# Kernel optimization log

Hardware: AMD Instinct MI355X
Metric: run time of the kernel (lower is better)

## Reference

```python
import jax, jax.numpy as jnp
import numpy as np

N_HEAD = 8
N_FEAT = 512
EPS = 1e-6


def _forward(query, Wq, bq, Wk, bk, Wv, bv, Wo, bo):
    # query: (bsz, tgt_len, E). key = value = query (self-attention).
    bsz, tgt_len, E = query.shape
    head_dim = E // N_HEAD
    n = bsz * N_HEAD

    # Faithful to torch: .view((L, N, E)) is a RESHAPE, not a transpose.
    x = query.reshape(tgt_len, bsz, E)

    q = x @ Wq.T + bq
    k = x @ Wk.T + bk
    v = x @ Wv.T + bv

    # relu activation on q, k (act_fun='relu')
    q = jax.nn.relu(q).reshape(tgt_len, n, head_dim).swapaxes(0, 1)  # (n, L, d)
    k = jax.nn.relu(k).reshape(tgt_len, n, head_dim).swapaxes(0, 1)  # (n, L, d)
    v = v.reshape(tgt_len, n, head_dim).swapaxes(0, 1)               # (n, L, d)

    # cos reweighting: weight_index = pi/2 * arange(1, m+1) / m
    m = tgt_len
    idx = (np.pi / 2) * jnp.arange(1, m + 1, dtype=query.dtype) / m  # (L,)
    idx = idx[None, :, None]                                         # (1, L, 1)
    q_ = jnp.concatenate([q * jnp.sin(idx), q * jnp.cos(idx)], axis=-1)  # (n, L, 2d)
    k_ = jnp.concatenate([k * jnp.sin(idx), k * jnp.cos(idx)], axis=-1)  # (n, L, 2d)

    # causal linear attention via cumsum recurrence
    kv = jnp.einsum('nld,nlm->nldm', k_, v)          # (n, L, 2d, d)
    kv_cum = jnp.cumsum(kv, axis=1)                  # (n, L, 2d, d)
    qkv = jnp.einsum('nld,nldm->nlm', q_, kv_cum)    # (n, L, d)
    k_cum = jnp.cumsum(k_, axis=1)                   # (n, L, 2d)
    denom = jnp.clip(jnp.einsum('nld,nld->nl', q_, k_cum), EPS, None)
    attn = qkv / denom[..., None]                    # (n, L, d)

    attn = attn.swapaxes(0, 1).reshape(tgt_len, bsz, E)
    out = attn @ Wo.T + bo
    # Faithful to torch: final .view back to (bsz, tgt_len, E) is a reshape.
    return out.reshape(bsz, tgt_len, N_FEAT)


def setup_inputs() -> dict:
    key = jax.random.key(0)
    ks = jax.random.split(key, 9)
    bsz, L, E = 2, 1024, N_FEAT
    scale = 0.02
    return {
        'query': jax.random.normal(ks[0], (bsz, L, E), dtype=jnp.float32),
        'Wq': jax.random.normal(ks[1], (E, E), dtype=jnp.float32) * scale,
        'bq': jnp.zeros((E,), dtype=jnp.float32),
        'Wk': jax.random.normal(ks[2], (E, E), dtype=jnp.float32) * scale,
        'bk': jnp.zeros((E,), dtype=jnp.float32),
        'Wv': jax.random.normal(ks[3], (E, E), dtype=jnp.float32) * scale,
        'bv': jnp.zeros((E,), dtype=jnp.float32),
        'Wo': jax.random.normal(ks[4], (E, E), dtype=jnp.float32) * scale,
        'bo': jnp.zeros((E,), dtype=jnp.float32),
    }


def reference(query, Wq, bq, Wk, bk, Wv, bv, Wo, bo):
    return _forward(query, Wq, bq, Wk, bk, Wv, bv, Wo, bo)
```

## Files before the change

kernel.cpp:

```cpp
#include <hip/hip_runtime.h>
#include <math.h>

#define LSEQ 1024
#define EDIM 512
#define HD 64
#define CCH 64
#define NCH 16
#define DFEAT 128

typedef unsigned short u16;
typedef short bf16x8 __attribute__((ext_vector_type(8)));
typedef float f32x4 __attribute__((ext_vector_type(4)));

__device__ __forceinline__ u16 f2bf(float f) {
    unsigned u = __float_as_uint(f);
    unsigned r = (u + 0x7fffu + ((u >> 16) & 1u)) >> 16;
    return (u16)r;
}
__device__ __forceinline__ float bf2f(u16 x) {
    return __uint_as_float((unsigned)x << 16);
}
__device__ __forceinline__ void async16(void* lds, const void* g) {
    __builtin_amdgcn_global_load_lds(
        (const __attribute__((address_space(1))) unsigned int*)g,
        (__attribute__((address_space(3))) unsigned int*)lds, 16, 0, 0);
}

__global__ __launch_bounds__(256) void cast_kernel(
    const float* __restrict__ X,  const float* __restrict__ Wq,
    const float* __restrict__ Wk, const float* __restrict__ Wv,
    const float* __restrict__ Wo, u16* __restrict__ Xb, u16* __restrict__ Wb)
{
    int i = blockIdx.x * 256 + threadIdx.x;
    const float* src; u16* dst; int off;
    if (i < 262144)      { src = X;  dst = Xb;          off = i; }
    else if (i < 327680) { src = Wq; dst = Wb;          off = i - 262144; }
    else if (i < 393216) { src = Wk; dst = Wb + 262144; off = i - 327680; }
    else if (i < 458752) { src = Wv; dst = Wb + 524288; off = i - 393216; }
    else                 { src = Wo; dst = Wb + 786432; off = i - 458752; }
    float4 v = *(const float4*)&src[(size_t)off * 4];
    ushort4 o; o.x = f2bf(v.x); o.y = f2bf(v.y); o.z = f2bf(v.z); o.w = f2bf(v.w);
    *(ushort4*)&dst[(size_t)off * 4] = o;
}

__global__ __launch_bounds__(256) void qkv_mfma_kernel(
    const u16* __restrict__ Xb, const u16* __restrict__ Wb,
    const float* __restrict__ bq, const float* __restrict__ bk, const float* __restrict__ bv,
    u16* __restrict__ qf, u16* __restrict__ kf, u16* __restrict__ vf)
{
    const int z = blockIdx.z;
    const u16* __restrict__ W = Wb + (size_t)z * 262144;
    const float* __restrict__ bias = (z == 0) ? bq : (z == 1) ? bk : bv;
    const int r0 = blockIdx.x * 128;
    const int j0 = blockIdx.y * 64;
    __shared__ u16 As[128 * 32];
    __shared__ u16 Bs[64 * 32];
    const int t = threadIdx.x;
    const int wave = t >> 6, lane = t & 63;
    const int cl = lane & 15, rg4 = lane >> 4;
    f32x4 acc[2][4];
    #pragma unroll
    for (int ri = 0; ri < 2; ++ri)
        #pragma unroll
        for (int cj = 0; cj < 4; ++cj) acc[ri][cj] = (f32x4){0.f, 0.f, 0.f, 0.f};

    for (int kb = 0; kb < 512; kb += 32) {
        #pragma unroll
        for (int i = 0; i < 2; ++i) {
            int chunk = i * 256 + t;
            int row = chunk >> 2, kg = chunk & 3;
            async16(&As[(i * 256 + wave * 64) * 8], Xb + (size_t)(r0 + row) * 512 + kb + kg * 8);
        }
        {
            int row = t >> 2, kg = t & 3;
            async16(&Bs[(wave * 64) * 8], W + (size_t)(j0 + row) * 512 + kb + kg * 8);
        }
        __syncthreads();
        bf16x8 af[2], bg[4];
        #pragma unroll
        for (int ri = 0; ri < 2; ++ri)
            af[ri] = *(const bf16x8*)&As[(wave * 32 + ri * 16 + cl) * 32 + rg4 * 8];
        #pragma unroll
        for (int cj = 0; cj < 4; ++cj)
            bg[cj] = *(const bf16x8*)&Bs[(cj * 16 + cl) * 32 + rg4 * 8];
        #pragma unroll
        for (int ri = 0; ri < 2; ++ri)
            #pragma unroll
            for (int cj = 0; cj < 4; ++cj)
                acc[ri][cj] = __builtin_amdgcn_mfma_f32_16x16x32_bf16(af[ri], bg[cj], acc[ri][cj], 0, 0, 0);
        __syncthreads();
    }

    float biasv[4];
    #pragma unroll
    for (int cj = 0; cj < 4; ++cj) biasv[cj] = bias[j0 + cj * 16 + cl];
    const int h = j0 >> 6;
    #pragma unroll
    for (int ri = 0; ri < 2; ++ri) {
        #pragma unroll
        for (int rr = 0; rr < 4; ++rr) {
            const int row_g = r0 + wave * 32 + ri * 16 + rg4 * 4 + rr;
            const int l = row_g >> 1, bb = row_g & 1;
            if (z < 2) {
                float ang = 1.5707963267948966f * (float)(l + 1) * (1.0f / 1024.0f);
                float sv, cv;
                sincosf(ang, &sv, &cv);
                u16* __restrict__ dst = (z == 0) ? qf : kf;
                size_t base = (size_t)((bb * 8 + h) * LSEQ + l) * DFEAT;
                #pragma unroll
                for (int cj = 0; cj < 4; ++cj) {
                    const int d = cj * 16 + cl;
                    float y = fmaxf(acc[ri][cj][rr] + biasv[cj], 0.f);
                    dst[base + d]      = f2bf(y * sv);
                    dst[base + d + 64] = f2bf(y * cv);
                }
            } else {
                size_t base = (size_t)((bb * 8 + h) * LSEQ + l) * HD;
                #pragma unroll
                for (int cj = 0; cj < 4; ++cj) {
                    const int d = cj * 16 + cl;
                    vf[base + d] = f2bf(acc[ri][cj][rr] + biasv[cj]);
                }
            }
        }
    }
}

__global__ __launch_bounds__(256) void chunk_sum_kernel(
    const u16* __restrict__ kf, const u16* __restrict__ vf,
    u16* __restrict__ KVc, float* __restrict__ K1c)
{
    const int n = blockIdx.x >> 4;
    const int c = blockIdx.x & 15;
    __shared__ u16 Ks[64 * 128];
    __shared__ u16 KT[128 * 68];
    __shared__ u16 Vs[64 * 64];
    __shared__ u16 VT[64 * 68];
    const int t = threadIdx.x;
    const int wave = t >> 6, lane = t & 63;
    const int cl = lane & 15, rg4 = lane >> 4;
    const u16* kbase = kf + (size_t)(n * LSEQ + c * CCH) * DFEAT;
    const u16* vbase = vf + (size_t)(n * LSEQ + c * CCH) * HD;
    #pragma unroll
    for (int i = 0; i < 4; ++i)
        async16(&Ks[(i * 256 + wave * 64) * 8], kbase + (size_t)(i * 256 + t) * 8);
    #pragma unroll
    for (int i = 0; i < 2; ++i)
        async16(&Vs[(i * 256 + wave * 64) * 8], vbase + (size_t)(i * 256 + t) * 8);
    __syncthreads();
    {
        int m = t & 63, l0 = (t >> 6) * 16;
        #pragma unroll
        for (int half = 0; half < 2; ++half) {
            u16 tmp[8];
            #pragma unroll
            for (int j = 0; j < 8; ++j) tmp[j] = Vs[(l0 + half * 8 + j) * 64 + m];
            *(bf16x8*)&VT[m * 68 + l0 + half * 8] = *(bf16x8*)tmp;
        }
    }
    {
        int d = t & 127, l0 = (t >> 7) * 32;
        #pragma unroll
        for (int q = 0; q < 4; ++q) {
            u16 tmp[8];
            #pragma unroll
            for (int j = 0; j < 8; ++j) tmp[j] = Ks[(l0 + q * 8 + j) * 128 + d];
            *(bf16x8*)&KT[d * 68 + l0 + q * 8] = *(bf16x8*)tmp;
        }
    }
    __syncthreads();
    bf16x8 af[2];
    #pragma unroll
    for (int ks = 0; ks < 2; ++ks)
        af[ks] = *(const bf16x8*)&VT[(wave * 16 + cl) * 68 + ks * 32 + rg4 * 8];
    u16* kvout = KVc + (size_t)(n * NCH + c) * (HD * DFEAT);
    #pragma unroll
    for (int dt = 0; dt < 8; ++dt) {
        f32x4 acc = (f32x4){0.f, 0.f, 0.f, 0.f};
        #pragma unroll
        for (int ks = 0; ks < 2; ++ks) {
            bf16x8 bfr = *(const bf16x8*)&KT[(dt * 16 + cl) * 68 + ks * 32 + rg4 * 8];
            acc = __builtin_amdgcn_mfma_f32_16x16x32_bf16(af[ks], bfr, acc, 0, 0, 0);
        }
        #pragma unroll
        for (int r = 0; r < 4; ++r)
            kvout[(size_t)(wave * 16 + rg4 * 4 + r) * 128 + dt * 16 + cl] = f2bf(acc[r]);
    }
    if (t < 128) {
        float s = 0.f;
        #pragma unroll
        for (int g = 0; g < 8; ++g) {
            bf16x8 kv = *(const bf16x8*)&KT[t * 68 + g * 8];
            #pragma unroll
            for (int j = 0; j < 8; ++j) s += bf2f(((u16*)&kv)[j]);
        }
        K1c[(size_t)(n * NCH + c) * DFEAT + t] = s;
    }
}

__global__ __launch_bounds__(256) void prefix_kernel(
    const u16* __restrict__ KVc, const float* __restrict__ K1c,
    u16* __restrict__ Spt, float* __restrict__ K1p)
{
    const int b = blockIdx.x, t = threadIdx.x;
    const int n = b >> 5;
    const int e = (b & 31) * 256 + t;
    const u16* src = KVc + (size_t)n * NCH * 8192 + e;
    u16* dst = Spt + (size_t)n * NCH * 8192 + e;
    float v[NCH];
    #pragma unroll
    for (int cc = 0; cc < NCH; ++cc) v[cc] = bf2f(src[(size_t)cc * 8192]);
    float run = 0.f;
    #pragma unroll
    for (int cc = 0; cc < NCH; ++cc) { dst[(size_t)cc * 8192] = f2bf(run); run += v[cc]; }
    if (b < 8) {
        const int idx = b * 256 + t;
        const int nn = idx >> 7, d = idx & 127;
        const float* s2 = K1c + (size_t)nn * NCH * DFEAT + d;
        float* d2 = K1p + (size_t)nn * NCH * DFEAT + d;
        float v2[NCH];
        #pragma unroll
        for (int cc = 0; cc < NCH; ++cc) v2[cc] = s2[cc * DFEAT];
        float run2 = 0.f;
        #pragma unroll
        for (int cc = 0; cc < NCH; ++cc) { d2[cc * DFEAT] = run2; run2 += v2[cc]; }
    }
}

__global__ __launch_bounds__(256) void attn_kernel(
    const u16* __restrict__ qf, const u16* __restrict__ kf, const u16* __restrict__ vf,
    const u16* __restrict__ Spt, const float* __restrict__ K1p,
    u16* __restrict__ Amb)
{
    const int n = blockIdx.x >> 4;
    const int c = blockIdx.x & 15;
    __shared__ u16 Qs[64 * 136];
    __shared__ u16 Ks[64 * 136];
    __shared__ u16 VT[64 * 68];
    __shared__ u16 Am[64 * 68];
    __shared__ float K1s[128];
    __shared__ float dsum[64];
    __shared__ float qk1[64];
    const int t = threadIdx.x;
    const int wave = t >> 6, lane = t & 63;
    const int cl = lane & 15, rg4 = lane >> 4;

    const u16* qbase = qf + (size_t)(n * LSEQ + c * CCH) * DFEAT;
    const u16* kbase = kf + (size_t)(n * LSEQ + c * CCH) * DFEAT;
    const u16* vbase = vf + (size_t)(n * LSEQ + c * CCH) * HD;
    const u16* spbase = Spt + (size_t)(n * NCH + c) * 8192;

    bf16x8 spf[4][4];
    #pragma unroll
    for (int nj = 0; nj < 4; ++nj)
        #pragma unroll
        for (int ks = 0; ks < 4; ++ks)
            spf[nj][ks] = *(const bf16x8*)&spbase[(nj * 16 + cl) * 128 + ks * 32 + rg4 * 8];

    #pragma unroll
    for (int i = 0; i < 4; ++i) {
        int chunk = i * 256 + t;
        int row = chunk >> 4, c8 = chunk & 15;
        *(bf16x8*)&Qs[row * 136 + c8 * 8] = *(const bf16x8*)&qbase[row * 128 + c8 * 8];
        *(bf16x8*)&Ks[row * 136 + c8 * 8] = *(const bf16x8*)&kbase[row * 128 + c8 * 8];
    }
    {
        #pragma unroll
        for (int half = 0; half < 2; ++half) {
            u16 tmp[8];
            #pragma unroll
            for (int j = 0; j < 8; ++j) tmp[j] = vbase[(wave * 16 + half * 8 + j) * HD + lane];
            *(bf16x8*)&VT[lane * 68 + wave * 16 + half * 8] = *(bf16x8*)tmp;
        }
    }
    if (t < 128) K1s[t] = K1p[(size_t)(n * NCH + c) * DFEAT + t];
    __syncthreads();

    f32x4 a_acc[4];
    #pragma unroll
    for (int nj = 0; nj < 4; ++nj) a_acc[nj] = (f32x4){0.f, 0.f, 0.f, 0.f};
    #pragma unroll
    for (int ks = 0; ks < 4; ++ks) {
        bf16x8 aq = *(const bf16x8*)&Qs[(wave * 16 + cl) * 136 + ks * 32 + rg4 * 8];
        #pragma unroll
        for (int nj = 0; nj < 4; ++nj) {
            bf16x8 bk = *(const bf16x8*)&Ks[(nj * 16 + cl) * 136 + ks * 32 + rg4 * 8];
            a_acc[nj] = __builtin_amdgcn_mfma_f32_16x16x32_bf16(aq, bk, a_acc[nj], 0, 0, 0);
        }
    }
    #pragma unroll
    for (int r = 0; r < 4; ++r) {
        int l_loc = wave * 16 + rg4 * 4 + r;
        float rs = 0.f;
        #pragma unroll
        for (int nj = 0; nj < 4; ++nj) {
            int lp = nj * 16 + cl;
            float v = (lp <= l_loc) ? a_acc[nj][r] : 0.f;
            Am[l_loc * 68 + lp] = f2bf(v);
            rs += v;
        }
        rs += __shfl_xor(rs, 1); rs += __shfl_xor(rs, 2);
        rs += __shfl_xor(rs, 4); rs += __shfl_xor(rs, 8);
        if (cl == 0) dsum[l_loc] = rs;
    }
    {
        int row = wave * 16 + (lane >> 2), seg = lane & 3;
        float s = 0.f;
        #pragma unroll
        for (int j = 0; j < 32; ++j) {
            int d = seg * 32 + j;
            s += bf2f(Qs[row * 136 + d]) * K1s[d];
        }
        s += __shfl_xor(s, 1); s += __shfl_xor(s, 2);
        if (seg == 0) qk1[row] = s;
    }
    __syncthreads();

    f32x4 oacc[4];
    #pragma unroll
    for (int nj = 0; nj < 4; ++nj) oacc[nj] = (f32x4){0.f, 0.f, 0.f, 0.f};
    #pragma unroll
    for (int ks = 0; ks < 4; ++ks) {
        bf16x8 aq = *(const bf16x8*)&Qs[(wave * 16 + cl) * 136 + ks * 32 + rg4 * 8];
        #pragma unroll
        for (int nj = 0; nj < 4; ++nj)
            oacc[nj] = __builtin_amdgcn_mfma_f32_16x16x32_bf16(aq, spf[nj][ks], oacc[nj], 0, 0, 0);
    }
    #pragma unroll
    for (int ks2 = 0; ks2 < 2; ++ks2) {
        bf16x8 aa = *(const bf16x8*)&Am[(wave * 16 + cl) * 68 + ks2 * 32 + rg4 * 8];
        #pragma unroll
        for (int nj = 0; nj < 4; ++nj) {
            bf16x8 bv = *(const bf16x8*)&VT[(nj * 16 + cl) * 68 + ks2 * 32 + rg4 * 8];
            oacc[nj] = __builtin_amdgcn_mfma_f32_16x16x32_bf16(aa, bv, oacc[nj], 0, 0, 0);
        }
    }
    const int bb = n >> 3, h = n & 7;
    #pragma unroll
    for (int r = 0; r < 4; ++r) {
        int l_loc = wave * 16 + rg4 * 4 + r;
        float den = fmaxf(dsum[l_loc] + qk1[l_loc], 1e-6f);
        float inv = 1.0f / den;
        int rrow = (c * CCH + l_loc) * 2 + bb;
        #pragma unroll
        for (int nj = 0; nj < 4; ++nj) {
            int m = nj * 16 + cl;
            Amb[(size_t)rrow * EDIM + h * 64 + m] = f2bf(oacc[nj][r] * inv);
        }
    }
}

__global__ __launch_bounds__(256) void out_mfma_kernel(
    const u16* __restrict__ Amb, const u16* __restrict__ Wob,
    const float* __restrict__ bo, float* __restrict__ out)
{
    const int r0 = blockIdx.x * 64;
    const int j0 = blockIdx.y * 64;
    __shared__ u16 As[64 * 32];
    __shared__ u16 Bs[64 * 32];
    const int t = threadIdx.x;
    const int wave = t >> 6, lane = t & 63;
    const int cl = lane & 15, rg4 = lane >> 4;
    f32x4 acc[4];
    #pragma unroll
    for (int cj = 0; cj < 4; ++cj) acc[cj] = (f32x4){0.f, 0.f, 0.f, 0.f};

    for (int kb = 0; kb < 512; kb += 32) {
        {
            int row = t >> 2, kg = t & 3;
            async16(&As[(wave * 64) * 8], Amb + (size_t)(r0 + row) * 512 + kb + kg * 8);
            async16(&Bs[(wave * 64) * 8], Wob + (size_t)(j0 + row) * 512 + kb + kg * 8);
        }
        __syncthreads();
        bf16x8 af = *(const bf16x8*)&As[(wave * 16 + cl) * 32 + rg4 * 8];
        bf16x8 bg[4];
        #pragma unroll
        for (int cj = 0; cj < 4; ++cj)
            bg[cj] = *(const bf16x8*)&Bs[(cj * 16 + cl) * 32 + rg4 * 8];
        #pragma unroll
        for (int cj = 0; cj < 4; ++cj)
            acc[cj] = __builtin_amdgcn_mfma_f32_16x16x32_bf16(af, bg[cj], acc[cj], 0, 0, 0);
        __syncthreads();
    }

    float bov[4];
    #pragma unroll
    for (int cj = 0; cj < 4; ++cj) bov[cj] = bo[j0 + cj * 16 + cl];
    #pragma unroll
    for (int rr = 0; rr < 4; ++rr) {
        const int row_g = r0 + wave * 16 + rg4 * 4 + rr;
        #pragma unroll
        for (int cj = 0; cj < 4; ++cj)
            out[(size_t)row_g * EDIM + j0 + cj * 16 + cl] = acc[cj][rr] + bov[cj];
    }
}

extern "C" void kernel_launch(void* const* d_in, const int* in_sizes, int n_in,
                              void* d_out, int out_size, void* d_ws, size_t ws_size,
                              hipStream_t stream) {
    const float* X  = (const float*)d_in[0];
    const float* Wq = (const float*)d_in[1]; const float* bq = (const float*)d_in[2];
    const float* Wk = (const float*)d_in[3]; const float* bk = (const float*)d_in[4];
    const float* Wv = (const float*)d_in[5]; const float* bv = (const float*)d_in[6];
    const float* Wo = (const float*)d_in[7]; const float* bo = (const float*)d_in[8];
    float* out = (float*)d_out;
    char* base = (char*)d_ws;
    u16*   qf  = (u16*)(base + 0);
    u16*   kf  = (u16*)(base + 4194304);
    u16*   vf  = (u16*)(base + 8388608);
    u16*   KVc = (u16*)(base + 10485760);
    float* K1c = (float*)(base + 14680064);
    u16*   Spt = (u16*)(base + 14811136);
    float* K1p = (float*)(base + 19005440);
    u16*   Amb = (u16*)(base + 19136512);
    u16*   Xb  = (u16*)(base + 21233664);
    u16*   Wb  = (u16*)(base + 23330816);

    hipLaunchKernelGGL(cast_kernel, dim3(2048), dim3(256), 0, stream,
                       X, Wq, Wk, Wv, Wo, Xb, Wb);
    hipLaunchKernelGGL(qkv_mfma_kernel, dim3(16, 8, 3), dim3(256), 0, stream,
                       Xb, Wb, bq, bk, bv, qf, kf, vf);
    hipLaunchKernelGGL(chunk_sum_kernel, dim3(256), dim3(256), 0, stream, kf, vf, KVc, K1c);
    hipLaunchKernelGGL(prefix_kernel, dim3(512), dim3(256), 0, stream, KVc, K1c, Spt, K1p);
    hipLaunchKernelGGL(attn_kernel, dim3(256), dim3(256), 0, stream,
                       qf, kf, vf, Spt, K1p, Amb);
    hipLaunchKernelGGL(out_mfma_kernel, dim3(32, 8), dim3(256), 0, stream,
                       Amb, Wb + 786432, bo, out);
}
```

Measured before the change: 110.1 us.

## Fold chunk prefix scan into attention kernel via per-chunk state MFMA accumulation

```diff
diff --git a/kernel.cpp b/kernel.cpp
--- a/kernel.cpp
+++ b/kernel.cpp
@@ -198,38 +198,9 @@
     }
 }
 
-__global__ __launch_bounds__(256) void prefix_kernel(
-    const u16* __restrict__ KVc, const float* __restrict__ K1c,
-    u16* __restrict__ Spt, float* __restrict__ K1p)
-{
-    const int b = blockIdx.x, t = threadIdx.x;
-    const int n = b >> 5;
-    const int e = (b & 31) * 256 + t;
-    const u16* src = KVc + (size_t)n * NCH * 8192 + e;
-    u16* dst = Spt + (size_t)n * NCH * 8192 + e;
-    float v[NCH];
-    #pragma unroll
-    for (int cc = 0; cc < NCH; ++cc) v[cc] = bf2f(src[(size_t)cc * 8192]);
-    float run = 0.f;
-    #pragma unroll
-    for (int cc = 0; cc < NCH; ++cc) { dst[(size_t)cc * 8192] = f2bf(run); run += v[cc]; }
-    if (b < 8) {
-        const int idx = b * 256 + t;
-        const int nn = idx >> 7, d = idx & 127;
-        const float* s2 = K1c + (size_t)nn * NCH * DFEAT + d;
-        float* d2 = K1p + (size_t)nn * NCH * DFEAT + d;
-        float v2[NCH];
-        #pragma unroll
-        for (int cc = 0; cc < NCH; ++cc) v2[cc] = s2[cc * DFEAT];
-        float run2 = 0.f;
-        #pragma unroll
-        for (int cc = 0; cc < NCH; ++cc) { d2[cc * DFEAT] = run2; run2 += v2[cc]; }
-    }
-}
-
 __global__ __launch_bounds__(256) void attn_kernel(
     const u16* __restrict__ qf, const u16* __restrict__ kf, const u16* __restrict__ vf,
-    const u16* __restrict__ Spt, const float* __restrict__ K1p,
+    const u16* __restrict__ KVc, const float* __restrict__ K1c,
     u16* __restrict__ Amb)
 {
     const int n = blockIdx.x >> 4;
@@ -248,14 +219,7 @@
     const u16* qbase = qf + (size_t)(n * LSEQ + c * CCH) * DFEAT;
     const u16* kbase = kf + (size_t)(n * LSEQ + c * CCH) * DFEAT;
     const u16* vbase = vf + (size_t)(n * LSEQ + c * CCH) * HD;
-    const u16* spbase = Spt + (size_t)(n * NCH + c) * 8192;
-
-    bf16x8 spf[4][4];
-    #pragma unroll
-    for (int nj = 0; nj < 4; ++nj)
-        #pragma unroll
-        for (int ks = 0; ks < 4; ++ks)
-            spf[nj][ks] = *(const bf16x8*)&spbase[(nj * 16 + cl) * 128 + ks * 32 + rg4 * 8];
+    const u16* kvbase = KVc + (size_t)n * NCH * 8192;
 
     #pragma unroll
     for (int i = 0; i < 4; ++i) {
@@ -273,19 +237,27 @@
             *(bf16x8*)&VT[lane * 68 + wave * 16 + half * 8] = *(bf16x8*)tmp;
         }
     }
-    if (t < 128) K1s[t] = K1p[(size_t)(n * NCH + c) * DFEAT + t];
+    if (t < 128) {
+        float s = 0.f;
+        for (int cc = 0; cc < c; ++cc) s += K1c[(size_t)(n * NCH + cc) * DFEAT + t];
+        K1s[t] = s;
+    }
     __syncthreads();
 
+    bf16x8 aq[4];
+    #pragma unroll
+    for (int ks = 0; ks < 4; ++ks)
+        aq[ks] = *(const bf16x8*)&Qs[(wave * 16 + cl) * 136 + ks * 32 + rg4 * 8];
+
     f32x4 a_acc[4];
     #pragma unroll
     for (int nj = 0; nj < 4; ++nj) a_acc[nj] = (f32x4){0.f, 0.f, 0.f, 0.f};
     #pragma unroll
     for (int ks = 0; ks < 4; ++ks) {
-        bf16x8 aq = *(const bf16x8*)&Qs[(wave * 16 + cl) * 136 + ks * 32 + rg4 * 8];
         #pragma unroll
         for (int nj = 0; nj < 4; ++nj) {
             bf16x8 bk = *(const bf16x8*)&Ks[(nj * 16 + cl) * 136 + ks * 32 + rg4 * 8];
-            a_acc[nj] = __builtin_amdgcn_mfma_f32_16x16x32_bf16(aq, bk, a_acc[nj], 0, 0, 0);
+            a_acc[nj] = __builtin_amdgcn_mfma_f32_16x16x32_bf16(aq[ks], bk, a_acc[nj], 0, 0, 0);
         }
     }
     #pragma unroll
@@ -319,12 +291,16 @@
     f32x4 oacc[4];
     #pragma unroll
     for (int nj = 0; nj < 4; ++nj) oacc[nj] = (f32x4){0.f, 0.f, 0.f, 0.f};
-    #pragma unroll
-    for (int ks = 0; ks < 4; ++ks) {
-        bf16x8 aq = *(const bf16x8*)&Qs[(wave * 16 + cl) * 136 + ks * 32 + rg4 * 8];
-        #pragma unroll
-        for (int nj = 0; nj < 4; ++nj)
-            oacc[nj] = __builtin_amdgcn_mfma_f32_16x16x32_bf16(aq, spf[nj][ks], oacc[nj], 0, 0, 0);
+    for (int cc = 0; cc < c; ++cc) {
+        const u16* sp = kvbase + (size_t)cc * 8192;
+        #pragma unroll
+        for (int ks = 0; ks < 4; ++ks) {
+            #pragma unroll
+            for (int nj = 0; nj < 4; ++nj) {
+                bf16x8 bv = *(const bf16x8*)&sp[(nj * 16 + cl) * 128 + ks * 32 + rg4 * 8];
+                oacc[nj] = __builtin_amdgcn_mfma_f32_16x16x32_bf16(aq[ks], bv, oacc[nj], 0, 0, 0);
+            }
+        }
     }
     #pragma unroll
     for (int ks2 = 0; ks2 < 2; ++ks2) {
@@ -410,20 +386,17 @@
     u16*   vf  = (u16*)(base + 8388608);
     u16*   KVc = (u16*)(base + 10485760);
     float* K1c = (float*)(base + 14680064);
-    u16*   Spt = (u16*)(base + 14811136);
-    float* K1p = (float*)(base + 19005440);
-    u16*   Amb = (u16*)(base + 19136512);
-    u16*   Xb  = (u16*)(base + 21233664);
-    u16*   Wb  = (u16*)(base + 23330816);
+    u16*   Amb = (u16*)(base + 14811136);
+    u16*   Xb  = (u16*)(base + 16908288);
+    u16*   Wb  = (u16*)(base + 19005440);
 
     hipLaunchKernelGGL(cast_kernel, dim3(2048), dim3(256), 0, stream,
                        X, Wq, Wk, Wv, Wo, Xb, Wb);
     hipLaunchKernelGGL(qkv_mfma_kernel, dim3(16, 8, 3), dim3(256), 0, stream,
                        Xb, Wb, bq, bk, bv, qf, kf, vf);
     hipLaunchKernelGGL(chunk_sum_kernel, dim3(256), dim3(256), 0, stream, kf, vf, KVc, K1c);
-    hipLaunchKernelGGL(prefix_kernel, dim3(512), dim3(256), 0, stream, KVc, K1c, Spt, K1p);
     hipLaunchKernelGGL(attn_kernel, dim3(256), dim3(256), 0, stream,
-                       qf, kf, vf, Spt, K1p, Amb);
+                       qf, kf, vf, KVc, K1c, Amb);
     hipLaunchKernelGGL(out_mfma_kernel, dim3(32, 8), dim3(256), 0, stream,
                        Amb, Wb + 786432, bo, out);
 }
```

Result: slower. 136.4 us (+23.9%).
